# Optimization experiments

Measured on AMD Instinct MI355X. Metric: run time of the kernel, lower is better.

## Reference

```python
import jax, jax.numpy as jnp
import numpy as np
from jax import lax


def log_g(x):
    # log of g(x) = x + 0.5 for x >= 0, sigmoid(x) for x < 0
    return jnp.where(x >= 0, jnp.log(jax.nn.relu(x) + 0.5), -jax.nn.softplus(-x))


def setup_inputs() -> dict:
    key = jax.random.key(0)
    k1, k2, k3, k4 = jax.random.split(key, 4)
    N, L, H_in, H = 8, 4096, 1024, 1024
    x = jax.random.normal(k1, (N, L, H_in), dtype=jnp.float32)
    W = jax.random.normal(k2, (2 * H, H_in), dtype=jnp.float32) * (1.0 / np.sqrt(H_in))
    b = jax.random.normal(k3, (2 * H,), dtype=jnp.float32) * 0.01
    hx = jax.random.uniform(k4, (N, H), dtype=jnp.float32)  # positive initial state
    return {"x": x, "W": W, "b": b, "hx": hx}


def reference(x, W, b, hx):
    # linear_ih: (N, L, 2H)
    zh = jnp.einsum('nli,oi->nlo', x, W) + b
    z, h_inter = jnp.split(zh, 2, axis=-1)  # each (N, L, H)
    log_z = -jax.nn.softplus(-z)            # log sigmoid(z)
    log_coeffs = -jax.nn.softplus(z)        # log (1 - sigmoid(z))
    log_h0 = jnp.log(hx)[:, None, :]        # (N, 1, H)
    log_tilde_h = log_g(h_inter)
    log_values = jnp.concatenate([log_h0, log_z + log_tilde_h], axis=1)  # (N, L+1, H)
    # Heinsen parallel scan in log space
    a_star = jnp.pad(jnp.cumsum(log_coeffs, axis=1), ((0, 0), (1, 0), (0, 0)))  # (N, L+1, H)
    log_h = a_star + lax.cumlogsumexp(log_values - a_star, axis=1)
    h = jnp.exp(log_h)
    return h[:, 1:]  # (N, L, H)
```

## Files before the change

kernel.cpp:

```cpp
#include <hip/hip_runtime.h>
#include <hip/hip_bf16.h>
#include <hip/hip_fp16.h>


#define N_B   8
#define L_SEQ 4096
#define H_DIM 1024
#define K_DIM 1024
#define O_DIM 2048
#define M_TOT (N_B * L_SEQ)

#define BM 128
#define BN 128
#define BK 64

#define NCHUNK 128
#define CLEN   (L_SEQ / NCHUNK)
#define NCH    (N_B * H_DIM)

typedef unsigned short ushort_t;
typedef unsigned short us8 __attribute__((ext_vector_type(8)));
typedef __bf16 v8bf __attribute__((ext_vector_type(8)));
typedef float f32x4 __attribute__((ext_vector_type(4)));

static __device__ __forceinline__ ushort_t f2bf(float f) {
    __hip_bfloat16 h = __float2bfloat16(f);
    return *reinterpret_cast<ushort_t*>(&h);
}

static __device__ __forceinline__ void dma16(const ushort_t* g, ushort_t* l) {
    __builtin_amdgcn_global_load_lds(
        (const __attribute__((address_space(1))) unsigned int*)g,
        (__attribute__((address_space(3))) unsigned int*)l,
        16, 0, 0);
}

__global__ __launch_bounds__(256) void cvt_f32_bf16(
    const float* __restrict__ src, ushort_t* __restrict__ dst)
{
    const int i = blockIdx.x * 256 + threadIdx.x;
    const float4 f0 = ((const float4*)src)[2 * i];
    const float4 f1 = ((const float4*)src)[2 * i + 1];
    us8 o;
    o[0] = f2bf(f0.x); o[1] = f2bf(f0.y); o[2] = f2bf(f0.z); o[3] = f2bf(f0.w);
    o[4] = f2bf(f1.x); o[5] = f2bf(f1.y); o[6] = f2bf(f1.z); o[7] = f2bf(f1.w);
    ((us8*)dst)[i] = o;
}

__global__ __launch_bounds__(256) void gemm_zh(
    const ushort_t* __restrict__ Xb,
    const ushort_t* __restrict__ Wb,
    const float* __restrict__ bias,
    __half* __restrict__ zbuf,
    __half* __restrict__ hbuf)
{
    __shared__ ushort_t As[BM * BK];
    __shared__ ushort_t Bs[BN * BK];

    const int tid    = threadIdx.x;
    const int wave   = tid >> 6;
    const int lane   = tid & 63;
    const int lane15 = lane & 15;
    const int quad   = lane >> 4;

    const int n0 = blockIdx.x * BN;
    const int m0 = blockIdx.y * BM;

    const int lrow = lane >> 3;
    const int jj   = (lane & 7) ^ lrow;
    const ushort_t* gA = Xb + (size_t)(m0 + wave * 8 + lrow) * K_DIM + jj * 8;
    const ushort_t* gB = Wb + (size_t)(n0 + wave * 8 + lrow) * K_DIM + jj * 8;
    ushort_t* lA = &As[(wave * 8) * BK];
    ushort_t* lB = &Bs[(wave * 8) * BK];

    const int wm = (wave >> 1) * 64;
    const int wn = (wave & 1) * 64;

    int offA[2][4], offB[2][4];
#pragma unroll
    for (int s = 0; s < 2; ++s) {
#pragma unroll
        for (int t = 0; t < 4; ++t) {
            const int rowA = wm + t * 16 + lane15;
            offA[s][t] = rowA * BK + (((s * 4 + quad) ^ (rowA & 7)) * 8);
            const int rowB = wn + t * 16 + lane15;
            offB[s][t] = rowB * BK + (((s * 4 + quad) ^ (rowB & 7)) * 8);
        }
    }

    const f32x4 fzero = {0.f, 0.f, 0.f, 0.f};
    f32x4 acc[4][4];
#pragma unroll
    for (int i = 0; i < 4; ++i)
#pragma unroll
        for (int j = 0; j < 4; ++j)
            acc[i][j] = fzero;

    for (int kt = 0; kt < K_DIM / BK; ++kt) {
        __syncthreads();
#pragma unroll
        for (int r = 0; r < 4; ++r) {
            dma16(gA + (size_t)r * 32 * K_DIM + kt * BK, lA + r * 32 * BK);
            dma16(gB + (size_t)r * 32 * K_DIM + kt * BK, lB + r * 32 * BK);
        }
        __syncthreads();

#pragma unroll
        for (int s = 0; s < 2; ++s) {
            v8bf af[4], bfr[4];
#pragma unroll
            for (int t = 0; t < 4; ++t) af[t]  = *(const v8bf*)(&As[offA[s][t]]);
#pragma unroll
            for (int t = 0; t < 4; ++t) bfr[t] = *(const v8bf*)(&Bs[offB[s][t]]);
#pragma unroll
            for (int i = 0; i < 4; ++i)
#pragma unroll
                for (int j = 0; j < 4; ++j)
                    acc[i][j] = __builtin_amdgcn_mfma_f32_16x16x32_bf16(
                        af[i], bfr[j], acc[i][j], 0, 0, 0);
        }
    }

    float bv[4];
#pragma unroll
    for (int j = 0; j < 4; ++j)
        bv[j] = bias[n0 + wn + j * 16 + lane15];

    __half* outb = (n0 < H_DIM) ? zbuf : hbuf;
    const int colbase = (n0 & (H_DIM - 1)) + wn + lane15;

#pragma unroll
    for (int i = 0; i < 4; ++i) {
#pragma unroll
        for (int r = 0; r < 4; ++r) {
            const size_t row = (size_t)(m0 + wm + i * 16 + quad * 4 + r);
            __half* p = outb + row * H_DIM + colbase;
#pragma unroll
            for (int j = 0; j < 4; ++j)
                p[j * 16] = __float2half(acc[i][j][r] + bv[j]);
        }
    }
}

__device__ __forceinline__ void gate_av(float z, float hi, float& a, float& v)
{
    const float e  = __expf(-z);
    const float sz = 1.0f / (1.0f + e);
    a = e * sz;
    const float g = (hi >= 0.0f) ? (hi + 0.5f)
                                 : (1.0f / (1.0f + __expf(-hi)));
    v = sz * g;
}

__global__ __launch_bounds__(256) void scan_phase1(
    const __half* __restrict__ zbuf, const __half* __restrict__ hbuf,
    float* __restrict__ Aar, float* __restrict__ Bar)
{
    const int idx = blockIdx.x * 256 + threadIdx.x;
    const int h8  = (idx & 127) << 3;
    const int n   = (idx >> 7) & 7;
    const int c   = idx >> 10;
    const size_t base = ((size_t)(n * L_SEQ + c * CLEN)) * H_DIM + h8;
    const float4* zp = (const float4*)(zbuf + base);
    const float4* hp = (const float4*)(hbuf + base);

    float A[8], B[8];
#pragma unroll
    for (int j = 0; j < 8; ++j) { A[j] = 1.f; B[j] = 0.f; }

#pragma unroll 4
    for (int s = 0; s < CLEN; ++s) {
        float4 zr = zp[(size_t)s * (H_DIM / 8)];
        float4 hr = hp[(size_t)s * (H_DIM / 8)];
        const __half2* z2 = (const __half2*)&zr;
        const __half2* i2 = (const __half2*)&hr;
#pragma unroll
        for (int j = 0; j < 4; ++j) {
            const float2 z  = __half22float2(z2[j]);
            const float2 hi = __half22float2(i2[j]);
            float a, v;
            gate_av(z.x, hi.x, a, v);
            B[2*j]   = fmaf(a, B[2*j],   v);  A[2*j]   *= a;
            gate_av(z.y, hi.y, a, v);
            B[2*j+1] = fmaf(a, B[2*j+1], v);  A[2*j+1] *= a;
        }
    }
    const size_t o = (size_t)c * NCH + n * H_DIM + h8;
    *(float4*)(Aar + o)     = *(const float4*)&A[0];
    *(float4*)(Aar + o + 4) = *(const float4*)&A[4];
    *(float4*)(Bar + o)     = *(const float4*)&B[0];
    *(float4*)(Bar + o + 4) = *(const float4*)&B[4];
}

__global__ __launch_bounds__(256) void scan_phase2(
    const float* __restrict__ Aar, const float* __restrict__ Bar,
    const float* __restrict__ hx, float* __restrict__ seed)
{
    const int ch = blockIdx.x * 256 + threadIdx.x;
    float carry = hx[ch];
#pragma unroll 8
    for (int c = 0; c < NCHUNK; ++c) {
        seed[c * NCH + ch] = carry;
        carry = fmaf(Aar[c * NCH + ch], carry, Bar[c * NCH + ch]);
    }
}

__global__ __launch_bounds__(256) void scan_phase3(
    const __half* __restrict__ zbuf, const __half* __restrict__ hbuf,
    const float* __restrict__ seed, float* __restrict__ out)
{
    const int idx = blockIdx.x * 256 + threadIdx.x;
    const int h8  = (idx & 127) << 3;
    const int n   = (idx >> 7) & 7;
    const int c   = idx >> 10;
    const size_t base = ((size_t)(n * L_SEQ + c * CLEN)) * H_DIM + h8;
    const float4* zp = (const float4*)(zbuf + base);
    const float4* hp = (const float4*)(hbuf + base);
    float* op = out + base;

    const size_t so = (size_t)c * NCH + n * H_DIM + h8;
    float h0[4], h1[4];
    *(float4*)h0 = *(const float4*)(seed + so);
    *(float4*)h1 = *(const float4*)(seed + so + 4);

#pragma unroll 4
    for (int s = 0; s < CLEN; ++s) {
        float4 zr = zp[(size_t)s * (H_DIM / 8)];
        float4 hr = hp[(size_t)s * (H_DIM / 8)];
        const __half2* z2 = (const __half2*)&zr;
        const __half2* i2 = (const __half2*)&hr;
#pragma unroll
        for (int j = 0; j < 2; ++j) {
            const float2 za = __half22float2(z2[j]);
            const float2 ia = __half22float2(i2[j]);
            float a, v;
            gate_av(za.x, ia.x, a, v);  h0[2*j]   = fmaf(a, h0[2*j],   v);
            gate_av(za.y, ia.y, a, v);  h0[2*j+1] = fmaf(a, h0[2*j+1], v);
            const float2 zb = __half22float2(z2[2+j]);
            const float2 ib = __half22float2(i2[2+j]);
            gate_av(zb.x, ib.x, a, v);  h1[2*j]   = fmaf(a, h1[2*j],   v);
            gate_av(zb.y, ib.y, a, v);  h1[2*j+1] = fmaf(a, h1[2*j+1], v);
        }
        float* pr = op + (size_t)s * H_DIM;
        *(float4*)pr       = *(const float4*)h0;
        *(float4*)(pr + 4) = *(const float4*)h1;
    }
}

extern "C" void kernel_launch(void* const* d_in, const int* in_sizes, int n_in,
                              void* d_out, int out_size, void* d_ws, size_t ws_size,
                              hipStream_t stream)
{
    const float* X    = (const float*)d_in[0];
    const float* Wm   = (const float*)d_in[1];
    const float* bias = (const float*)d_in[2];
    const float* hx   = (const float*)d_in[3];
    float* out = (float*)d_out;

    char* ws = (char*)d_ws;
    ushort_t* wb = (ushort_t*)ws;
    __half* zbuf = (__half*)(ws + (size_t)O_DIM * K_DIM * 2);
    __half* hbuf = zbuf + (size_t)M_TOT * H_DIM;
    float*  seed = (float*)(hbuf + (size_t)M_TOT * H_DIM);

    ushort_t* xb = (ushort_t*)d_out;
    float* Aar = out + (size_t)M_TOT * H_DIM / 2;
    float* Bar = Aar + (size_t)NCHUNK * NCH;

    cvt_f32_bf16<<<O_DIM * K_DIM / 8 / 256, 256, 0, stream>>>(Wm, wb);
    cvt_f32_bf16<<<M_TOT * K_DIM / 8 / 256, 256, 0, stream>>>(X, xb);

    dim3 ggrid(O_DIM / BN, M_TOT / BM);
    gemm_zh<<<ggrid, 256, 0, stream>>>(xb, wb, bias, zbuf, hbuf);

    const int p13_blocks = (NCH / 8) * NCHUNK / 256;
    scan_phase1<<<p13_blocks, 256, 0, stream>>>(zbuf, hbuf, Aar, Bar);
    scan_phase2<<<NCH / 256, 256, 0, stream>>>(Aar, Bar, hx, seed);
    scan_phase3<<<p13_blocks, 256, 0, stream>>>(zbuf, hbuf, seed, out);
}
```

Baseline: 476.9 us.

## Double scan chunk count, store seeds in fp16, use nontemporal output stores

```diff
diff --git a/kernel.cpp b/kernel.cpp
--- a/kernel.cpp
+++ b/kernel.cpp
@@ -14,7 +14,7 @@
 #define BN 128
 #define BK 64
 
-#define NCHUNK 128
+#define NCHUNK 256
 #define CLEN   (L_SEQ / NCHUNK)
 #define NCH    (N_B * H_DIM)
 
@@ -161,17 +161,17 @@
     const int n   = (idx >> 7) & 7;
     const int c   = idx >> 10;
     const size_t base = ((size_t)(n * L_SEQ + c * CLEN)) * H_DIM + h8;
-    const float4* zp = (const float4*)(zbuf + base);
-    const float4* hp = (const float4*)(hbuf + base);
+    const f32x4* zp = (const f32x4*)(zbuf + base);
+    const f32x4* hp = (const f32x4*)(hbuf + base);
 
     float A[8], B[8];
 #pragma unroll
     for (int j = 0; j < 8; ++j) { A[j] = 1.f; B[j] = 0.f; }
 
-#pragma unroll 4
+#pragma unroll
     for (int s = 0; s < CLEN; ++s) {
-        float4 zr = zp[(size_t)s * (H_DIM / 8)];
-        float4 hr = hp[(size_t)s * (H_DIM / 8)];
+        f32x4 zr = zp[(size_t)s * (H_DIM / 8)];
+        f32x4 hr = hp[(size_t)s * (H_DIM / 8)];
         const __half2* z2 = (const __half2*)&zr;
         const __half2* i2 = (const __half2*)&hr;
 #pragma unroll
@@ -186,47 +186,54 @@
         }
     }
     const size_t o = (size_t)c * NCH + n * H_DIM + h8;
-    *(float4*)(Aar + o)     = *(const float4*)&A[0];
-    *(float4*)(Aar + o + 4) = *(const float4*)&A[4];
-    *(float4*)(Bar + o)     = *(const float4*)&B[0];
-    *(float4*)(Bar + o + 4) = *(const float4*)&B[4];
+    *(f32x4*)(Aar + o)     = *(const f32x4*)&A[0];
+    *(f32x4*)(Aar + o + 4) = *(const f32x4*)&A[4];
+    *(f32x4*)(Bar + o)     = *(const f32x4*)&B[0];
+    *(f32x4*)(Bar + o + 4) = *(const f32x4*)&B[4];
 }
 
 __global__ __launch_bounds__(256) void scan_phase2(
     const float* __restrict__ Aar, const float* __restrict__ Bar,
-    const float* __restrict__ hx, float* __restrict__ seed)
+    const float* __restrict__ hx, __half* __restrict__ seed)
 {
     const int ch = blockIdx.x * 256 + threadIdx.x;
     float carry = hx[ch];
 #pragma unroll 8
     for (int c = 0; c < NCHUNK; ++c) {
-        seed[c * NCH + ch] = carry;
+        seed[c * NCH + ch] = __float2half(carry);
         carry = fmaf(Aar[c * NCH + ch], carry, Bar[c * NCH + ch]);
     }
 }
 
 __global__ __launch_bounds__(256) void scan_phase3(
     const __half* __restrict__ zbuf, const __half* __restrict__ hbuf,
-    const float* __restrict__ seed, float* __restrict__ out)
+    const __half* __restrict__ seed, float* __restrict__ out)
 {
     const int idx = blockIdx.x * 256 + threadIdx.x;
     const int h8  = (idx & 127) << 3;
     const int n   = (idx >> 7) & 7;
     const int c   = idx >> 10;
     const size_t base = ((size_t)(n * L_SEQ + c * CLEN)) * H_DIM + h8;
-    const float4* zp = (const float4*)(zbuf + base);
-    const float4* hp = (const float4*)(hbuf + base);
+    const f32x4* zp = (const f32x4*)(zbuf + base);
+    const f32x4* hp = (const f32x4*)(hbuf + base);
     float* op = out + base;
 
     const size_t so = (size_t)c * NCH + n * H_DIM + h8;
+    f32x4 sr = *(const f32x4*)(seed + so);
+    const __half2* s2 = (const __half2*)&sr;
     float h0[4], h1[4];
-    *(float4*)h0 = *(const float4*)(seed + so);
-    *(float4*)h1 = *(const float4*)(seed + so + 4);
-
-#pragma unroll 4
+#pragma unroll
+    for (int j = 0; j < 2; ++j) {
+        const float2 a = __half22float2(s2[j]);
+        h0[2*j] = a.x; h0[2*j+1] = a.y;
+        const float2 b = __half22float2(s2[2+j]);
+        h1[2*j] = b.x; h1[2*j+1] = b.y;
+    }
+
+#pragma unroll
     for (int s = 0; s < CLEN; ++s) {
-        float4 zr = zp[(size_t)s * (H_DIM / 8)];
-        float4 hr = hp[(size_t)s * (H_DIM / 8)];
+        f32x4 zr = zp[(size_t)s * (H_DIM / 8)];
+        f32x4 hr = hp[(size_t)s * (H_DIM / 8)];
         const __half2* z2 = (const __half2*)&zr;
         const __half2* i2 = (const __half2*)&hr;
 #pragma unroll
@@ -242,8 +249,8 @@
             gate_av(zb.y, ib.y, a, v);  h1[2*j+1] = fmaf(a, h1[2*j+1], v);
         }
         float* pr = op + (size_t)s * H_DIM;
-        *(float4*)pr       = *(const float4*)h0;
-        *(float4*)(pr + 4) = *(const float4*)h1;
+        __builtin_nontemporal_store(*(const f32x4*)h0, (f32x4*)pr);
+        __builtin_nontemporal_store(*(const f32x4*)h1, (f32x4*)(pr + 4));
     }
 }
 
@@ -261,7 +268,7 @@
     ushort_t* wb = (ushort_t*)ws;
     __half* zbuf = (__half*)(ws + (size_t)O_DIM * K_DIM * 2);
     __half* hbuf = zbuf + (size_t)M_TOT * H_DIM;
-    float*  seed = (float*)(hbuf + (size_t)M_TOT * H_DIM);
+    __half* seed = hbuf + (size_t)M_TOT * H_DIM;
 
     ushort_t* xb = (ushort_t*)d_out;
     float* Aar = out + (size_t)M_TOT * H_DIM / 2;
```

Measured after the change: 514.6 us. +7.9%, slower.
